# Kernel tuning notes

Measured on AMD Instinct MI355X. Metric: run time of the kernel, lower is better.

Reference implementation:

```python
import jax, jax.numpy as jnp
import numpy as np

T, D, E, I, TOP_K = 2048, 2048, 8, 2048, 2
SOFTCAP = 30.0


def setup_inputs() -> dict:
    key = jax.random.key(0)
    ks = jax.random.split(key, 5)
    s = 0.02  # realistic init scale
    return {
        "x": jax.random.normal(ks[0], (T, D), dtype=jnp.float32),
        "w_gate": jax.random.normal(ks[1], (E, D), dtype=jnp.float32) * s,
        "w1": jax.random.normal(ks[2], (E, I, D), dtype=jnp.float32) * s,
        "w3": jax.random.normal(ks[3], (E, I, D), dtype=jnp.float32) * s,
        "w2": jax.random.normal(ks[4], (E, D, I), dtype=jnp.float32) * s,
        "top_k": TOP_K,
    }


def reference(x, w_gate, w1, w3, w2, top_k):
    # Router gating linear in fp32 (ReplicatedLinear, bias=False)
    logits = jnp.einsum("td,ed->te", x.astype(jnp.float32), w_gate)  # [T,E]
    # Softcapped routing logits: cap * tanh(logits / cap)
    logits = SOFTCAP * jnp.tanh(logits / SOFTCAP)
    probs = jax.nn.softmax(logits, axis=-1)                          # [T,E]
    vals, idx = jax.lax.top_k(probs, top_k)                          # [T,k]
    num_experts = w_gate.shape[0]
    # Dense combine weights: zeros except top-k softmax probs (no renorm, Grok-1 style)
    combine = (jax.nn.one_hot(idx, num_experts, dtype=probs.dtype) * vals[..., None]).sum(axis=1)  # [T,E]
    combine = combine.astype(x.dtype)
    # Grok GLU experts: gelu(x@w1^T) * (x@w3^T) @ w2^T, evaluated per expert
    a = jnp.einsum("td,eid->tei", x, w1)  # [T,E,I]
    b = jnp.einsum("td,eid->tei", x, w3)
    h = jax.nn.gelu(a, approximate=False) * b
    y = jnp.einsum("tei,edi->ted", h, w2)  # [T,E,D]
    out = jnp.einsum("te,ted->td", combine, y)
    return out
```

## Files before the change

### kernel.cpp

```cpp
#include <hip/hip_runtime.h>
#include <hip/hip_bf16.h>
#include <math.h>

#define TT 2048
#define DD 2048
#define EE 8
#define II 2048
#define SOFTCAP 30.0f

typedef __attribute__((ext_vector_type(8))) short short8;
typedef __attribute__((ext_vector_type(4))) float f32x4;
typedef unsigned short u16;

__device__ __forceinline__ u16 f2bs(float f) {
    union { __hip_bfloat16 h; u16 u; } cv;
    cv.h = __float2bfloat16(f);
    return cv.u;
}

__device__ __forceinline__ void st_bf4(u16* p, float4 v) {
    unsigned int lo = (unsigned int)f2bs(v.x) | ((unsigned int)f2bs(v.y) << 16);
    unsigned int hi = (unsigned int)f2bs(v.z) | ((unsigned int)f2bs(v.w) << 16);
    *(uint2*)p = make_uint2(lo, hi);
}

__device__ __forceinline__ void gload16(const void* g, void* l) {
    __builtin_amdgcn_global_load_lds(
        (const __attribute__((address_space(1))) unsigned int*)g,
        (__attribute__((address_space(3))) unsigned int*)l,
        16, 0, 0);
}

__global__ __launch_bounds__(256) void cvt3_kernel(
    const float* __restrict__ w1, const float* __restrict__ w3,
    const float* __restrict__ w2, u16* __restrict__ d1, u16* __restrict__ d3,
    u16* __restrict__ d2, long long n)
{
    const float* s;
    u16* d;
    if (blockIdx.y == 0)      { s = w1; d = d1; }
    else if (blockIdx.y == 1) { s = w3; d = d3; }
    else                      { s = w2; d = d2; }
    long long i = ((long long)blockIdx.x * 256 + threadIdx.x) * 8;
    if (i >= n) return;
    float4 a = *(const float4*)(s + i);
    float4 b = *(const float4*)(s + i + 4);
    st_bf4(d + i, a);
    st_bf4(d + i + 4, b);
}

__global__ __launch_bounds__(256) void router2_kernel(
    const float* __restrict__ x, const float* __restrict__ wg,
    int* __restrict__ counts, int* __restrict__ list, float* __restrict__ wlist,
    u16* __restrict__ xb)
{
    const int wid = threadIdx.x >> 6;
    const int lane = threadIdx.x & 63;
    const int t = blockIdx.x * 4 + wid;
    const float* xr = x + (size_t)t * DD;
    float acc[EE];
#pragma unroll
    for (int e = 0; e < EE; ++e) acc[e] = 0.f;
    for (int i = 0; i < DD; i += 256) {
        float4 xv = *(const float4*)(xr + i + lane * 4);
        if (xb) st_bf4(xb + (size_t)t * DD + i + lane * 4, xv);
#pragma unroll
        for (int e = 0; e < EE; ++e) {
            float4 wv = *(const float4*)(wg + (size_t)e * DD + i + lane * 4);
            acc[e] += xv.x * wv.x + xv.y * wv.y + xv.z * wv.z + xv.w * wv.w;
        }
    }
#pragma unroll
    for (int e = 0; e < EE; ++e) {
#pragma unroll
        for (int off = 32; off > 0; off >>= 1)
            acc[e] += __shfl_xor(acc[e], off, 64);
    }
    if (lane == 0) {
        float p[EE];
        float mx = -1e30f;
#pragma unroll
        for (int e = 0; e < EE; ++e) {
            p[e] = SOFTCAP * tanhf(acc[e] / SOFTCAP);
            mx = fmaxf(mx, p[e]);
        }
        float s = 0.f;
#pragma unroll
        for (int e = 0; e < EE; ++e) { p[e] = expf(p[e] - mx); s += p[e]; }
        float inv = 1.f / s;
        int i0 = 0;
#pragma unroll
        for (int e = 1; e < EE; ++e) if (p[e] > p[i0]) i0 = e;
        int i1 = (i0 == 0) ? 1 : 0;
#pragma unroll
        for (int e = 0; e < EE; ++e) if (e != i0 && p[e] > p[i1]) i1 = e;
        int pos0 = atomicAdd(&counts[i0], 1);
        list[i0 * TT + pos0] = t * 2;
        wlist[i0 * TT + pos0] = p[i0] * inv;
        int pos1 = atomicAdd(&counts[i1], 1);
        list[i1 * TT + pos1] = t * 2 + 1;
        wlist[i1 * TT + pos1] = p[i1] * inv;
    }
}


__global__ __launch_bounds__(256) void gemm_h_bf16(
    const u16* __restrict__ xb, const u16* __restrict__ w1b,
    const u16* __restrict__ w3b, const int* __restrict__ counts,
    const int* __restrict__ list, const float* __restrict__ wlist,
    u16* __restrict__ H)
{
    const int e = blockIdx.z;
    const int cnt = counts[e];
    const int m0 = blockIdx.y * 128;
    if (m0 >= cnt) return;
    const int n0 = blockIdx.x * 64;
    const int tid = threadIdx.x;
    const int lane = tid & 63;
    const int w = tid >> 6;

    __shared__ u16 As[2][128 * 32];
    __shared__ u16 W1s[2][64 * 32];
    __shared__ u16 W3s[2][64 * 32];

    const int colb = ((lane & 3) ^ ((lane >> 3) & 3)) * 8;
    const int rsub = lane >> 2;
    const int rA0 = w * 16 + rsub;
    const int rA1 = 64 + rA0;
    const int mA0 = m0 + rA0, mA1 = m0 + rA1;
    const int t0 = (mA0 < cnt) ? (list[e * TT + mA0] >> 1) : 0;
    const int t1 = (mA1 < cnt) ? (list[e * TT + mA1] >> 1) : 0;
    const u16* gA0 = xb + (size_t)t0 * DD + colb;
    const u16* gA1 = xb + (size_t)t1 * DD + colb;
    const int rW = w * 16 + rsub;
    const u16* gW1 = w1b + ((size_t)e * II + n0 + rW) * DD + colb;
    const u16* gW3 = w3b + ((size_t)e * II + n0 + rW) * DD + colb;

    const int wm = w >> 1, wn = w & 1;
    const int lr = lane & 15;
    const int quad = lane >> 4;
    const int qc = (quad ^ ((lr >> 1) & 3)) * 8;

    f32x4 accA[4][2], accB[4][2];
#pragma unroll
    for (int mi = 0; mi < 4; ++mi)
#pragma unroll
        for (int ni = 0; ni < 2; ++ni) {
            accA[mi][ni] = (f32x4)0.f;
            accB[mi][ni] = (f32x4)0.f;
        }

#define STAGE_H(b, kk) do { \
    gload16(gA0 + (kk), &As[b][(w * 16) * 32]); \
    gload16(gA1 + (kk), &As[b][(64 + w * 16) * 32]); \
    gload16(gW1 + (kk), &W1s[b][(w * 16) * 32]); \
    gload16(gW3 + (kk), &W3s[b][(w * 16) * 32]); \
} while (0)

    STAGE_H(0, 0);
    __syncthreads();
    for (int it = 0; it < DD / 32; ++it) {
        const int cur = it & 1;
        if (it + 1 < DD / 32) STAGE_H(cur ^ 1, (it + 1) * 32);

        short8 af[4], b1f[2], b3f[2];
#pragma unroll
        for (int mi = 0; mi < 4; ++mi)
            af[mi] = *(const short8*)&As[cur][(wm * 64 + mi * 16 + lr) * 32 + qc];
#pragma unroll
        for (int ni = 0; ni < 2; ++ni) {
            b1f[ni] = *(const short8*)&W1s[cur][(wn * 32 + ni * 16 + lr) * 32 + qc];
            b3f[ni] = *(const short8*)&W3s[cur][(wn * 32 + ni * 16 + lr) * 32 + qc];
        }
#pragma unroll
        for (int mi = 0; mi < 4; ++mi)
#pragma unroll
            for (int ni = 0; ni < 2; ++ni) {
                accA[mi][ni] = __builtin_amdgcn_mfma_f32_16x16x32_bf16(af[mi], b1f[ni], accA[mi][ni], 0, 0, 0);
                accB[mi][ni] = __builtin_amdgcn_mfma_f32_16x16x32_bf16(af[mi], b3f[ni], accB[mi][ni], 0, 0, 0);
            }
        __syncthreads();
    }
#undef STAGE_H

#pragma unroll
    for (int mi = 0; mi < 4; ++mi) {
#pragma unroll
        for (int reg = 0; reg < 4; ++reg) {
            int m = m0 + wm * 64 + mi * 16 + quad * 4 + reg;
            if (m < cnt) {
                int entry = list[e * TT + m];
                float cw = wlist[e * TT + m];
                size_t hbase = (size_t)entry * II;
#pragma unroll
                for (int ni = 0; ni < 2; ++ni) {
                    int col = n0 + wn * 32 + ni * 16 + lr;
                    float a = accA[mi][ni][reg];
                    float b = accB[mi][ni][reg];
                    float g = 0.5f * a * (1.0f + erff(a * 0.70710678118654752f));
                    H[hbase + col] = f2bs(g * b * cw);
                }
            }
        }
    }
}

__global__ __launch_bounds__(256) void gemm_y_bf16(
    const u16* __restrict__ H, const u16* __restrict__ w2b,
    const int* __restrict__ counts, const int* __restrict__ list,
    float* __restrict__ Y)
{
    const int e = blockIdx.z;
    const int cnt = counts[e];
    const int m0 = blockIdx.y * 128;
    if (m0 >= cnt) return;
    const int n0 = blockIdx.x * 128;
    const int tid = threadIdx.x;
    const int lane = tid & 63;
    const int w = tid >> 6;

    __shared__ u16 As[2][128 * 32];
    __shared__ u16 Bs[2][128 * 32];

    const int colb = ((lane & 3) ^ ((lane >> 3) & 3)) * 8;
    const int rsub = lane >> 2;
    const int rA0 = w * 16 + rsub;
    const int rA1 = 64 + rA0;
    const int eA0 = (m0 + rA0 < cnt) ? list[e * TT + m0 + rA0] : 0;
    const int eA1 = (m0 + rA1 < cnt) ? list[e * TT + m0 + rA1] : 0;
    const u16* gA0 = H + (size_t)eA0 * II + colb;
    const u16* gA1 = H + (size_t)eA1 * II + colb;
    const u16* gB0 = w2b + ((size_t)e * DD + n0 + rA0) * II + colb;
    const u16* gB1 = w2b + ((size_t)e * DD + n0 + rA1) * II + colb;

    const int wm = w >> 1, wn = w & 1;
    const int lr = lane & 15;
    const int quad = lane >> 4;
    const int qc = (quad ^ ((lr >> 1) & 3)) * 8;

    f32x4 acc[4][4];
#pragma unroll
    for (int mi = 0; mi < 4; ++mi)
#pragma unroll
        for (int ni = 0; ni < 4; ++ni) acc[mi][ni] = (f32x4)0.f;

#define STAGE_Y(b, kk) do { \
    gload16(gA0 + (kk), &As[b][(w * 16) * 32]); \
    gload16(gA1 + (kk), &As[b][(64 + w * 16) * 32]); \
    gload16(gB0 + (kk), &Bs[b][(w * 16) * 32]); \
    gload16(gB1 + (kk), &Bs[b][(64 + w * 16) * 32]); \
} while (0)

    STAGE_Y(0, 0);
    __syncthreads();
    for (int it = 0; it < II / 32; ++it) {
        const int cur = it & 1;
        if (it + 1 < II / 32) STAGE_Y(cur ^ 1, (it + 1) * 32);

        short8 af[4], bf[4];
#pragma unroll
        for (int mi = 0; mi < 4; ++mi)
            af[mi] = *(const short8*)&As[cur][(wm * 64 + mi * 16 + lr) * 32 + qc];
#pragma unroll
        for (int ni = 0; ni < 4; ++ni)
            bf[ni] = *(const short8*)&Bs[cur][(wn * 64 + ni * 16 + lr) * 32 + qc];
#pragma unroll
        for (int mi = 0; mi < 4; ++mi)
#pragma unroll
            for (int ni = 0; ni < 4; ++ni)
                acc[mi][ni] = __builtin_amdgcn_mfma_f32_16x16x32_bf16(af[mi], bf[ni], acc[mi][ni], 0, 0, 0);
        __syncthreads();
    }
#undef STAGE_Y

#pragma unroll
    for (int mi = 0; mi < 4; ++mi) {
#pragma unroll
        for (int reg = 0; reg < 4; ++reg) {
            int m = m0 + wm * 64 + mi * 16 + quad * 4 + reg;
            if (m < cnt) {
                int entry = list[e * TT + m];
                float* yrow = Y + (size_t)entry * DD + n0 + wn * 64;
#pragma unroll
                for (int ni = 0; ni < 4; ++ni)
                    yrow[ni * 16 + lr] = acc[mi][ni][reg];
            }
        }
    }
}

__global__ __launch_bounds__(256) void combine_kernel(
    const float* __restrict__ Y, float* __restrict__ out)
{
    long long i4 = ((long long)blockIdx.x * 256 + threadIdx.x) * 4;
    int t = (int)(i4 >> 11);
    int d = (int)(i4 & 2047);
    float4 a = *(const float4*)(Y + (size_t)(2 * t) * DD + d);
    float4 b = *(const float4*)(Y + (size_t)(2 * t + 1) * DD + d);
    float4 r = make_float4(a.x + b.x, a.y + b.y, a.z + b.z, a.w + b.w);
    *(float4*)(out + i4) = r;
}

__global__ __launch_bounds__(256) void gemm_h_fb(
    const float* __restrict__ x, const float* __restrict__ w1,
    const float* __restrict__ w3, const int* __restrict__ counts,
    const int* __restrict__ list, const float* __restrict__ wlist,
    __hip_bfloat16* __restrict__ H)
{
    const int e = blockIdx.z;
    const int cnt = counts[e];
    const int m0 = blockIdx.y * 128;
    if (m0 >= cnt) return;
    const int n0 = blockIdx.x * 64;
    const int tid = threadIdx.x;

    __shared__ u16 As[128][40];
    __shared__ u16 W1s[64][40];
    __shared__ u16 W3s[64][40];

    const int arow = tid >> 1;
    const int ahalf = tid & 1;
    const bool avalid = (m0 + arow) < cnt;
    const float* aptr = nullptr;
    if (avalid) {
        int entry = list[e * TT + m0 + arow];
        aptr = x + (size_t)(entry >> 1) * DD + ahalf * 16;
    }
    const int wrow = tid >> 2;
    const int wq = tid & 3;
    const float* w1ptr = w1 + ((size_t)e * II + (n0 + wrow)) * DD + wq * 8;
    const float* w3ptr = w3 + ((size_t)e * II + (n0 + wrow)) * DD + wq * 8;

    const int lane = tid & 63;
    const int wid = tid >> 6;
    const int wm = wid >> 1;
    const int wn = wid & 1;
    const int lr = lane & 15;
    const int quad = lane >> 4;

    f32x4 accA[4][2], accB[4][2];
#pragma unroll
    for (int mi = 0; mi < 4; ++mi)
#pragma unroll
        for (int ni = 0; ni < 2; ++ni) {
            accA[mi][ni] = (f32x4)0.f;
            accB[mi][ni] = (f32x4)0.f;
        }

    for (int kk = 0; kk < DD; kk += 32) {
#pragma unroll
        for (int it = 0; it < 4; ++it) {
            float4 v = make_float4(0.f, 0.f, 0.f, 0.f);
            if (avalid) v = *(const float4*)(aptr + kk + it * 4);
            st_bf4(&As[arow][ahalf * 16 + it * 4], v);
        }
#pragma unroll
        for (int it = 0; it < 2; ++it) {
            float4 v1 = *(const float4*)(w1ptr + kk + it * 4);
            st_bf4(&W1s[wrow][wq * 8 + it * 4], v1);
            float4 v3 = *(const float4*)(w3ptr + kk + it * 4);
            st_bf4(&W3s[wrow][wq * 8 + it * 4], v3);
        }
        __syncthreads();

        short8 af[4], b1f[2], b3f[2];
#pragma unroll
        for (int mi = 0; mi < 4; ++mi)
            af[mi] = *(const short8*)&As[wm * 64 + mi * 16 + lr][quad * 8];
#pragma unroll
        for (int ni = 0; ni < 2; ++ni) {
            b1f[ni] = *(const short8*)&W1s[wn * 32 + ni * 16 + lr][quad * 8];
            b3f[ni] = *(const short8*)&W3s[wn * 32 + ni * 16 + lr][quad * 8];
        }
#pragma unroll
        for (int mi = 0; mi < 4; ++mi)
#pragma unroll
            for (int ni = 0; ni < 2; ++ni) {
                accA[mi][ni] = __builtin_amdgcn_mfma_f32_16x16x32_bf16(af[mi], b1f[ni], accA[mi][ni], 0, 0, 0);
                accB[mi][ni] = __builtin_amdgcn_mfma_f32_16x16x32_bf16(af[mi], b3f[ni], accB[mi][ni], 0, 0, 0);
            }
        __syncthreads();
    }

#pragma unroll
    for (int mi = 0; mi < 4; ++mi) {
#pragma unroll
        for (int reg = 0; reg < 4; ++reg) {
            int m = m0 + wm * 64 + mi * 16 + quad * 4 + reg;
            if (m < cnt) {
                int entry = list[e * TT + m];
                float cw = wlist[e * TT + m];
                size_t hbase = (size_t)entry * II;
#pragma unroll
                for (int ni = 0; ni < 2; ++ni) {
                    int col = n0 + wn * 32 + ni * 16 + lr;
                    float a = accA[mi][ni][reg];
                    float b = accB[mi][ni][reg];
                    float g = 0.5f * a * (1.0f + erff(a * 0.70710678118654752f));
                    H[hbase + col] = __float2bfloat16(g * b * cw);
                }
            }
        }
    }
}

__global__ __launch_bounds__(256) void gemm_y_fb(
    const __hip_bfloat16* __restrict__ H, const float* __restrict__ w2,
    const int* __restrict__ counts, const int* __restrict__ list,
    float* __restrict__ out)
{
    const int e = blockIdx.z;
    const int cnt = counts[e];
    const int m0 = blockIdx.y * 128;
    if (m0 >= cnt) return;
    const int n0 = blockIdx.x * 128;
    const int tid = threadIdx.x;

    __shared__ u16 As[128][40];
    __shared__ u16 Ws[128][40];

    const int arow = tid >> 1;
    const int ahalf = tid & 1;
    const bool avalid = (m0 + arow) < cnt;
    const u16* aptr = nullptr;
    if (avalid) {
        int entry = list[e * TT + m0 + arow];
        aptr = (const u16*)H + (size_t)entry * II + ahalf * 16;
    }
    const int wrow = tid >> 1;
    const int whalf = tid & 1;
    const float* wptr = w2 + ((size_t)e * DD + (n0 + wrow)) * II + whalf * 16;

    const int lane = tid & 63;
    const int wid = tid >> 6;
    const int wm = wid >> 1;
    const int wn = wid & 1;
    const int lr = lane & 15;
    const int quad = lane >> 4;

    f32x4 acc[4][4];
#pragma unroll
    for (int mi = 0; mi < 4; ++mi)
#pragma unroll
        for (int ni = 0; ni < 4; ++ni) acc[mi][ni] = (f32x4)0.f;

    for (int kk = 0; kk < II; kk += 32) {
#pragma unroll
        for (int it = 0; it < 2; ++it) {
            int4 v = make_int4(0, 0, 0, 0);
            if (avalid) v = *(const int4*)(aptr + kk + it * 8);
            *(int4*)&As[arow][ahalf * 16 + it * 8] = v;
        }
#pragma unroll
        for (int it = 0; it < 4; ++it) {
            float4 v = *(const float4*)(wptr + kk + it * 4);
            st_bf4(&Ws[wrow][whalf * 16 + it * 4], v);
        }
        __syncthreads();

        short8 af[4], bf[4];
#pragma unroll
        for (int mi = 0; mi < 4; ++mi)
            af[mi] = *(const short8*)&As[wm * 64 + mi * 16 + lr][quad * 8];
#pragma unroll
        for (int ni = 0; ni < 4; ++ni)
            bf[ni] = *(const short8*)&Ws[wn * 64 + ni * 16 + lr][quad * 8];
#pragma unroll
        for (int mi = 0; mi < 4; ++mi)
#pragma unroll
            for (int ni = 0; ni < 4; ++ni)
                acc[mi][ni] = __builtin_amdgcn_mfma_f32_16x16x32_bf16(af[mi], bf[ni], acc[mi][ni], 0, 0, 0);
        __syncthreads();
    }

#pragma unroll
    for (int mi = 0; mi < 4; ++mi) {
#pragma unroll
        for (int reg = 0; reg < 4; ++reg) {
            int m = m0 + wm * 64 + mi * 16 + quad * 4 + reg;
            if (m < cnt) {
                int token = list[e * TT + m] >> 1;
                float* orow = out + (size_t)token * DD + n0 + wn * 64;
#pragma unroll
                for (int ni = 0; ni < 4; ++ni)
                    atomicAdd(&orow[ni * 16 + lr], acc[mi][ni][reg]);
            }
        }
    }
}

extern "C" void kernel_launch(void* const* d_in, const int* in_sizes, int n_in,
                              void* d_out, int out_size, void* d_ws, size_t ws_size,
                              hipStream_t stream) {
    const float* x  = (const float*)d_in[0];
    const float* wg = (const float*)d_in[1];
    const float* w1 = (const float*)d_in[2];
    const float* w3 = (const float*)d_in[3];
    const float* w2 = (const float*)d_in[4];
    float* out = (float*)d_out;

    char* ws = (char*)d_ws;
    int*   counts = (int*)(ws);
    int*   list   = (int*)(ws + 4096);
    float* wlist  = (float*)(ws + 4096 + 65536);
    u16*   H      = (u16*)(ws + 135168);
    const size_t NW = (size_t)EE * II * DD;
    u16*   xb  = (u16*)(ws + 135168 + 16777216);
    u16*   w1b = (u16*)((char*)xb + (size_t)TT * DD * 2);
    u16*   w3b = (u16*)((char*)w1b + NW * 2);
    u16*   w2b = (u16*)((char*)w3b + NW * 2);
    float* Y = (float*)xb;
    const size_t NEED = (size_t)135168 + 16777216 + (size_t)TT * DD * 2 + 3 * NW * 2;

    hipMemsetAsync(counts, 0, EE * sizeof(int), stream);

    if (ws_size >= NEED) {
        router2_kernel<<<TT / 4, 256, 0, stream>>>(x, wg, counts, list, wlist, xb);
        const int cvb = (int)(NW / 8 / 256);
        cvt3_kernel<<<dim3(cvb, 3), 256, 0, stream>>>(w1, w3, w2, w1b, w3b, w2b, (long long)NW);
        gemm_h_bf16<<<dim3(II / 64, TT / 128, EE), 256, 0, stream>>>(
            xb, w1b, w3b, counts, list, wlist, H);
        gemm_y_bf16<<<dim3(DD / 128, TT / 128, EE), 256, 0, stream>>>(
            H, w2b, counts, list, Y);
        combine_kernel<<<(TT * DD / 4) / 256, 256, 0, stream>>>(Y, out);
    } else {
        hipMemsetAsync(out, 0, (size_t)out_size * sizeof(float), stream);
        router2_kernel<<<TT / 4, 256, 0, stream>>>(x, wg, counts, list, wlist, nullptr);
        gemm_h_fb<<<dim3(II / 64, TT / 128, EE), 256, 0, stream>>>(
            x, w1, w3, counts, list, wlist, (__hip_bfloat16*)H);
        gemm_y_fb<<<dim3(DD / 128, TT / 128, EE), 256, 0, stream>>>(
            (const __hip_bfloat16*)H, w2, counts, list, out);
    }
}
```

Before: 677.2 us.

## Deepen GEMM shared-memory pipeline to four stages with explicit waitcnt scheduling

```diff
diff --git a/kernel.cpp b/kernel.cpp
--- a/kernel.cpp
+++ b/kernel.cpp
@@ -38,9 +38,9 @@
 {
     const float* s;
     u16* d;
-    if (blockIdx.y == 0)      { s = w1; d = d1; }
-    else if (blockIdx.y == 1) { s = w3; d = d3; }
-    else                      { s = w2; d = d2; }
+    if (blockIdx.y == 0)      { s = w2; d = d2; }
+    else if (blockIdx.y == 1) { s = w1; d = d1; }
+    else                      { s = w3; d = d3; }
     long long i = ((long long)blockIdx.x * 256 + threadIdx.x) * 8;
     if (i >= n) return;
     float4 a = *(const float4*)(s + i);
@@ -103,6 +103,8 @@
     }
 }
 
+
+#define SB0 __builtin_amdgcn_sched_barrier(0)
 
 __global__ __launch_bounds__(256) void gemm_h_bf16(
     const u16* __restrict__ xb, const u16* __restrict__ w1b,
@@ -119,9 +121,9 @@
     const int lane = tid & 63;
     const int w = tid >> 6;
 
-    __shared__ u16 As[2][128 * 32];
-    __shared__ u16 W1s[2][64 * 32];
-    __shared__ u16 W3s[2][64 * 32];
+    __shared__ u16 As[4][128 * 32];
+    __shared__ u16 W1s[4][64 * 32];
+    __shared__ u16 W3s[4][64 * 32];
 
     const int colb = ((lane & 3) ^ ((lane >> 3) & 3)) * 8;
     const int rsub = lane >> 2;
@@ -150,37 +152,59 @@
             accB[mi][ni] = (f32x4)0.f;
         }
 
-#define STAGE_H(b, kk) do { \
-    gload16(gA0 + (kk), &As[b][(w * 16) * 32]); \
-    gload16(gA1 + (kk), &As[b][(64 + w * 16) * 32]); \
-    gload16(gW1 + (kk), &W1s[b][(w * 16) * 32]); \
-    gload16(gW3 + (kk), &W3s[b][(w * 16) * 32]); \
+#define STAGE_H(u, kk) do { \
+    gload16(gA0 + (kk), &As[u][(w * 16) * 32]); \
+    gload16(gA1 + (kk), &As[u][(64 + w * 16) * 32]); \
+    gload16(gW1 + (kk), &W1s[u][(w * 16) * 32]); \
+    gload16(gW3 + (kk), &W3s[u][(w * 16) * 32]); \
 } while (0)
 
+#define HSTEP(u, j, VM, DOSTAGE) do { \
+    asm volatile("s_waitcnt vmcnt(" #VM ")" ::: "memory"); \
+    SB0; \
+    __builtin_amdgcn_s_barrier(); \
+    SB0; \
+    short8 af[4], b1f[2], b3f[2]; \
+    _Pragma("unroll") \
+    for (int mi = 0; mi < 4; ++mi) \
+        af[mi] = *(const short8*)&As[u][(wm * 64 + mi * 16 + lr) * 32 + qc]; \
+    _Pragma("unroll") \
+    for (int ni = 0; ni < 2; ++ni) { \
+        b1f[ni] = *(const short8*)&W1s[u][(wn * 32 + ni * 16 + lr) * 32 + qc]; \
+        b3f[ni] = *(const short8*)&W3s[u][(wn * 32 + ni * 16 + lr) * 32 + qc]; \
+    } \
+    SB0; \
+    asm volatile("s_waitcnt lgkmcnt(0)" ::: "memory"); \
+    SB0; \
+    __builtin_amdgcn_s_barrier(); \
+    SB0; \
+    if (DOSTAGE) STAGE_H(u, ((j) + 4) * 32); \
+    _Pragma("unroll") \
+    for (int mi = 0; mi < 4; ++mi) \
+        _Pragma("unroll") \
+        for (int ni = 0; ni < 2; ++ni) { \
+            accA[mi][ni] = __builtin_amdgcn_mfma_f32_16x16x32_bf16(af[mi], b1f[ni], accA[mi][ni], 0, 0, 0); \
+            accB[mi][ni] = __builtin_amdgcn_mfma_f32_16x16x32_bf16(af[mi], b3f[ni], accB[mi][ni], 0, 0, 0); \
+        } \
+} while (0)
+
     STAGE_H(0, 0);
-    __syncthreads();
-    for (int it = 0; it < DD / 32; ++it) {
-        const int cur = it & 1;
-        if (it + 1 < DD / 32) STAGE_H(cur ^ 1, (it + 1) * 32);
-
-        short8 af[4], b1f[2], b3f[2];
-#pragma unroll
-        for (int mi = 0; mi < 4; ++mi)
-            af[mi] = *(const short8*)&As[cur][(wm * 64 + mi * 16 + lr) * 32 + qc];
-#pragma unroll
-        for (int ni = 0; ni < 2; ++ni) {
-            b1f[ni] = *(const short8*)&W1s[cur][(wn * 32 + ni * 16 + lr) * 32 + qc];
-            b3f[ni] = *(const short8*)&W3s[cur][(wn * 32 + ni * 16 + lr) * 32 + qc];
-        }
-#pragma unroll
-        for (int mi = 0; mi < 4; ++mi)
-#pragma unroll
-            for (int ni = 0; ni < 2; ++ni) {
-                accA[mi][ni] = __builtin_amdgcn_mfma_f32_16x16x32_bf16(af[mi], b1f[ni], accA[mi][ni], 0, 0, 0);
-                accB[mi][ni] = __builtin_amdgcn_mfma_f32_16x16x32_bf16(af[mi], b3f[ni], accB[mi][ni], 0, 0, 0);
-            }
-        __syncthreads();
-    }
+    STAGE_H(1, 32);
+    STAGE_H(2, 64);
+    STAGE_H(3, 96);
+
+    for (int g = 0; g < 15; ++g) {
+        const int j = g * 4;
+        HSTEP(0, j + 0, 12, true);
+        HSTEP(1, j + 1, 12, true);
+        HSTEP(2, j + 2, 12, true);
+        HSTEP(3, j + 3, 12, true);
+    }
+    HSTEP(0, 60, 12, false);
+    HSTEP(1, 61, 8, false);
+    HSTEP(2, 62, 4, false);
+    HSTEP(3, 63, 0, false);
+#undef HSTEP
 #undef STAGE_H
 
 #pragma unroll
@@ -197,8 +221,8 @@
                     int col = n0 + wn * 32 + ni * 16 + lr;
                     float a = accA[mi][ni][reg];
                     float b = accB[mi][ni][reg];
-                    float g = 0.5f * a * (1.0f + erff(a * 0.70710678118654752f));
-                    H[hbase + col] = f2bs(g * b * cw);
+                    float g2 = 0.5f * a * (1.0f + erff(a * 0.70710678118654752f));
+                    H[hbase + col] = f2bs(g2 * b * cw);
                 }
             }
         }
@@ -219,8 +243,8 @@
     const int lane = tid & 63;
     const int w = tid >> 6;
 
-    __shared__ u16 As[2][128 * 32];
-    __shared__ u16 Bs[2][128 * 32];
+    __shared__ u16 As[4][128 * 32];
+    __shared__ u16 Bs[4][128 * 32];
 
     const int colb = ((lane & 3) ^ ((lane >> 3) & 3)) * 8;
     const int rsub = lane >> 2;
@@ -244,33 +268,55 @@
 #pragma unroll
         for (int ni = 0; ni < 4; ++ni) acc[mi][ni] = (f32x4)0.f;
 
-#define STAGE_Y(b, kk) do { \
-    gload16(gA0 + (kk), &As[b][(w * 16) * 32]); \
-    gload16(gA1 + (kk), &As[b][(64 + w * 16) * 32]); \
-    gload16(gB0 + (kk), &Bs[b][(w * 16) * 32]); \
-    gload16(gB1 + (kk), &Bs[b][(64 + w * 16) * 32]); \
+#define STAGE_Y(u, kk) do { \
+    gload16(gA0 + (kk), &As[u][(w * 16) * 32]); \
+    gload16(gA1 + (kk), &As[u][(64 + w * 16) * 32]); \
+    gload16(gB0 + (kk), &Bs[u][(w * 16) * 32]); \
+    gload16(gB1 + (kk), &Bs[u][(64 + w * 16) * 32]); \
 } while (0)
 
+#define YSTEP(u, j, VM, DOSTAGE) do { \
+    asm volatile("s_waitcnt vmcnt(" #VM ")" ::: "memory"); \
+    SB0; \
+    __builtin_amdgcn_s_barrier(); \
+    SB0; \
+    short8 af[4], bf[4]; \
+    _Pragma("unroll") \
+    for (int mi = 0; mi < 4; ++mi) \
+        af[mi] = *(const short8*)&As[u][(wm * 64 + mi * 16 + lr) * 32 + qc]; \
+    _Pragma("unroll") \
+    for (int ni = 0; ni < 4; ++ni) \
+        bf[ni] = *(const short8*)&Bs[u][(wn * 64 + ni * 16 + lr) * 32 + qc]; \
+    SB0; \
+    asm volatile("s_waitcnt lgkmcnt(0)" ::: "memory"); \
+    SB0; \
+    __builtin_amdgcn_s_barrier(); \
+    SB0; \
+    if (DOSTAGE) STAGE_Y(u, ((j) + 4) * 32); \
+    _Pragma("unroll") \
+    for (int mi = 0; mi < 4; ++mi) \
+        _Pragma("unroll") \
+        for (int ni = 0; ni < 4; ++ni) \
+            acc[mi][ni] = __builtin_amdgcn_mfma_f32_16x16x32_bf16(af[mi], bf[ni], acc[mi][ni], 0, 0, 0); \
+} while (0)
+
     STAGE_Y(0, 0);
-    __syncthreads();
-    for (int it = 0; it < II / 32; ++it) {
-        const int cur = it & 1;
-        if (it + 1 < II / 32) STAGE_Y(cur ^ 1, (it + 1) * 32);
-
-        short8 af[4], bf[4];
-#pragma unroll
-        for (int mi = 0; mi < 4; ++mi)
-            af[mi] = *(const short8*)&As[cur][(wm * 64 + mi * 16 + lr) * 32 + qc];
-#pragma unroll
-        for (int ni = 0; ni < 4; ++ni)
-            bf[ni] = *(const short8*)&Bs[cur][(wn * 64 + ni * 16 + lr) * 32 + qc];
-#pragma unroll
-        for (int mi = 0; mi < 4; ++mi)
-#pragma unroll
-            for (int ni = 0; ni < 4; ++ni)
-                acc[mi][ni] = __builtin_amdgcn_mfma_f32_16x16x32_bf16(af[mi], bf[ni], acc[mi][ni], 0, 0, 0);
-        __syncthreads();
-    }
+    STAGE_Y(1, 32);
+    STAGE_Y(2, 64);
+    STAGE_Y(3, 96);
+
+    for (int g = 0; g < 15; ++g) {
+        const int j = g * 4;
+        YSTEP(0, j + 0, 12, true);
+        YSTEP(1, j + 1, 12, true);
+        YSTEP(2, j + 2, 12, true);
+        YSTEP(3, j + 3, 12, true);
+    }
+    YSTEP(0, 60, 12, false);
+    YSTEP(1, 61, 8, false);
+    YSTEP(2, 62, 4, false);
+    YSTEP(3, 63, 0, false);
+#undef YSTEP
 #undef STAGE_Y
 
 #pragma unroll
```

New measurement: 684.5 us. About the same (+1.1%).
